# Kernel optimization log

Measured on AMD Instinct MI355X. Metric: run time of the kernel, lower is better.

Reference implementation:

```python
import jax, jax.numpy as jnp
import numpy as np

B, T, C, NH = 4, 2048, 1024, 16
HD = C // NH  # head dim = 64


def setup_inputs() -> dict:
    key = jax.random.key(0)
    k1, k2, k3 = jax.random.split(key, 3)
    x = jax.random.normal(k1, (B, T, C), dtype=jnp.float32)
    w_attn = jax.random.normal(k2, (C, 3 * C), dtype=jnp.float32) * (1.0 / np.sqrt(C))
    b_attn = jnp.zeros((3 * C,), dtype=jnp.float32)
    w_proj = jax.random.normal(k3, (C, C), dtype=jnp.float32) * (1.0 / np.sqrt(C))
    b_proj = jnp.zeros((C,), dtype=jnp.float32)
    return {"x": x, "w_attn": w_attn, "b_attn": b_attn, "w_proj": w_proj, "b_proj": b_proj}


def reference(x, w_attn, b_attn, w_proj, b_proj):
    Bx, Tx, Cx = x.shape
    # fused QKV projection
    qkv = x @ w_attn + b_attn              # [B, T, 3C]
    q, k, v = jnp.split(qkv, 3, axis=-1)   # each [B, T, C]
    # split heads: [B, NH, T, HD]
    q = q.reshape(Bx, Tx, NH, HD).transpose(0, 2, 1, 3)
    k = k.reshape(Bx, Tx, NH, HD).transpose(0, 2, 1, 3)
    v = v.reshape(Bx, Tx, NH, HD).transpose(0, 2, 1, 3)
    scale = 1.0 / np.sqrt(HD)
    att = jnp.einsum('bhqd,bhkd->bhqk', q, k) * scale  # [B, NH, T, T]
    causal = jnp.tril(jnp.ones((Tx, Tx), dtype=bool))
    att = jnp.where(causal[None, None], att, -jnp.inf)
    att = jax.nn.softmax(att, axis=-1)
    y = jnp.einsum('bhqk,bhkd->bhqd', att, v)           # [B, NH, T, HD]
    y = y.transpose(0, 2, 1, 3).reshape(Bx, Tx, Cx)
    return y @ w_proj + b_proj
```

## Files before the change

### kernel.cpp

```cpp
#include <hip/hip_runtime.h>
#include <hip/hip_bf16.h>

#define B_SZ 4
#define T_SZ 2048
#define C_SZ 1024
#define NH_SZ 16
#define HD_SZ 64
#define M_SZ (B_SZ * T_SZ)

typedef __bf16 bf16x8 __attribute__((ext_vector_type(8)));
typedef __bf16 bf16x4 __attribute__((ext_vector_type(4)));
typedef float f32x4 __attribute__((ext_vector_type(4)));

__device__ __forceinline__ void async_ld16(__hip_bfloat16* lds, const __hip_bfloat16* g) {
  __builtin_amdgcn_global_load_lds(
      (const __attribute__((address_space(1))) void*)g,
      (__attribute__((address_space(3))) void*)lds, 16, 0, 0);
}

__device__ __forceinline__ void bar() {
  asm volatile("" ::: "memory");
  __builtin_amdgcn_s_barrier();
  asm volatile("" ::: "memory");
}

__device__ __forceinline__ bf16x8 frag32(const __hip_bfloat16* base, int row, int q) {
  const int byte = (row << 6) + (((q ^ (row >> 1)) & 3) << 4);
  return *(const bf16x8*)((const char*)base + byte);
}

#define SWZ(row, cb) (((row) << 7) + ((cb) ^ (((row) & 7) << 4)))

__device__ __forceinline__ uint32_t pk2(float lo, float hi) {
  uint32_t r;
  asm("v_cvt_pk_bf16_f32 %0, %1, %2" : "=v"(r) : "v"(lo), "v"(hi));
  return r;
}

__global__ __launch_bounds__(256) void conv_bf16_kernel(
    const float* __restrict__ X, __hip_bfloat16* __restrict__ Y) {
  const int i = (blockIdx.x * 256 + threadIdx.x) * 4;
  float4 v = *(const float4*)&X[i];
  union { bf16x4 v; __hip_bfloat16 h[4]; } o;
  o.h[0] = __float2bfloat16(v.x); o.h[1] = __float2bfloat16(v.y);
  o.h[2] = __float2bfloat16(v.z); o.h[3] = __float2bfloat16(v.w);
  *(bf16x4*)&Y[i] = o.v;
}

template <int KD, int ND>
__global__ __launch_bounds__(256) void transpose_conv_kernel(
    const float* __restrict__ W, __hip_bfloat16* __restrict__ Wt) {
  __shared__ float sT[32][33];
  const int n0 = blockIdx.x * 32, k0 = blockIdx.y * 32;
  const int tid = threadIdx.x;
  {
    const int r = tid >> 3, c = (tid & 7) * 4;
    float4 v = *(const float4*)&W[(size_t)(k0 + r) * ND + n0 + c];
    sT[r][c] = v.x; sT[r][c + 1] = v.y; sT[r][c + 2] = v.z; sT[r][c + 3] = v.w;
  }
  __syncthreads();
  {
    const int n = tid >> 3, kq = (tid & 7) * 4;
    union { bf16x4 v; __hip_bfloat16 h[4]; } o;
#pragma unroll
    for (int j = 0; j < 4; ++j) o.h[j] = __float2bfloat16(sT[kq + j][n]);
    *(bf16x4*)&Wt[(size_t)(n0 + n) * KD + k0 + kq] = o.v;
  }
}


#define Q_PRESCALE 0.18033688011112042f

__global__ __launch_bounds__(512, 4) void gemm_qk_ring(
    const __hip_bfloat16* __restrict__ A, const __hip_bfloat16* __restrict__ Bt,
    const float* __restrict__ bias,
    __hip_bfloat16* __restrict__ qR, __hip_bfloat16* __restrict__ kR) {
  __shared__ __align__(16) __hip_bfloat16 sA[3][256 * 32];
  __shared__ __align__(16) __hip_bfloat16 sB[3][128 * 32];

  const int tid = threadIdx.x;
  const int wave = tid >> 6, lane = tid & 63;
  const int quad = lane >> 4, l16 = lane & 15;
  const int wm = wave >> 1, wn = wave & 1;

  const int xcd = (int)blockIdx.x & 7, lb = (int)blockIdx.x >> 3;
  const int bm = (xcd * 4 + (lb >> 4)) * 256;
  const int bn = (lb & 15) * 128;

  const int srow = tid >> 2;
  const int scol = 8 * ((tid & 3) ^ ((tid >> 3) & 3));
  const int sdst = tid * 8;
  const __hip_bfloat16* gA = A + (size_t)(bm + srow) * C_SZ + scol;
  const __hip_bfloat16* gB = Bt + (size_t)(bn + srow) * C_SZ + scol;

  f32x4 acc[4][4];
#pragma unroll
  for (int i = 0; i < 4; ++i)
#pragma unroll
    for (int j = 0; j < 4; ++j) acc[i][j] = (f32x4){0.f, 0.f, 0.f, 0.f};

#define STGQK(buf, kt)                                                         \
  do {                                                                         \
    async_ld16(&sA[buf][sdst], gA + (kt) * 32);                                \
    async_ld16(&sA[buf][4096 + sdst], gA + (size_t)128 * C_SZ + (kt) * 32);    \
    async_ld16(&sB[buf][sdst], gB + (kt) * 32);                                \
  } while (0)

  STGQK(0, 0);
  STGQK(1, 1);
  asm volatile("s_waitcnt vmcnt(3)" ::: "memory");
  bar();

  constexpr int NT = C_SZ / 32;
  int cur = 0;
  for (int kt = 0; kt < NT; ++kt) {
    const int stg = cur == 0 ? 2 : cur - 1;
    if (kt + 2 < NT) STGQK(stg, kt + 2);

    const __hip_bfloat16* ab = sA[cur];
    const __hip_bfloat16* bb = sB[cur];
    bf16x8 af[4], bfr[4];
#pragma unroll
    for (int mq = 0; mq < 4; ++mq) af[mq] = frag32(ab, wm * 64 + mq * 16 + l16, quad);
#pragma unroll
    for (int nq = 0; nq < 4; ++nq) bfr[nq] = frag32(bb, wn * 64 + nq * 16 + l16, quad);
#pragma unroll
    for (int mq = 0; mq < 4; ++mq)
#pragma unroll
      for (int nq = 0; nq < 4; ++nq)
        acc[mq][nq] = __builtin_amdgcn_mfma_f32_16x16x32_bf16(af[mq], bfr[nq], acc[mq][nq], 0, 0, 0);

    if (kt + 1 < NT) {
      if (kt + 2 < NT) asm volatile("s_waitcnt vmcnt(3)" ::: "memory");
      else             asm volatile("s_waitcnt vmcnt(0)" ::: "memory");
      bar();
    }
    cur = cur == 2 ? 0 : cur + 1;
  }
#undef STGQK

  float bv[4];
#pragma unroll
  for (int nq = 0; nq < 4; ++nq) bv[nq] = bias[bn + wn * 64 + nq * 16 + l16];
  const bool isQ = bn < C_SZ;
#pragma unroll
  for (int mq = 0; mq < 4; ++mq)
#pragma unroll
    for (int nq = 0; nq < 4; ++nq) {
      const int col = bn + wn * 64 + nq * 16 + l16;
      const int hh = (col >> 6) & 15, d = col & 63;
#pragma unroll
      for (int r = 0; r < 4; ++r) {
        const int row = bm + wm * 64 + mq * 16 + quad * 4 + r;
        const int bb_ = row >> 11, t = row & 2047;
        const size_t idx = ((size_t)(bb_ * 16 + hh) * T_SZ + t) * HD_SZ + d;
        const float val = acc[mq][nq][r] + bv[nq];
        if (isQ) qR[idx] = __float2bfloat16(val * Q_PRESCALE);
        else     kR[idx] = __float2bfloat16(val);
      }
    }
}

template <int MODE>
__global__ __launch_bounds__(256, 3) void gemm_tri128(
    const __hip_bfloat16* __restrict__ A, const __hip_bfloat16* __restrict__ Bt,
    const float* __restrict__ bias, float* __restrict__ Cf,
    __hip_bfloat16* __restrict__ vT) {
  __shared__ __align__(16) __hip_bfloat16 sA[3][128 * 32];
  __shared__ __align__(16) __hip_bfloat16 sB[3][128 * 32];

  const int tid = threadIdx.x;
  const int wave = tid >> 6, lane = tid & 63;
  const int quad = lane >> 4, l16 = lane & 15;
  const int rw = (wave & 1) * 64, cw = (wave >> 1) * 64;

  const int xcd = (int)blockIdx.x & 7, lb = (int)blockIdx.x >> 3;
  const int bm = (xcd * 8 + (lb >> 3)) * 128;
  const int bn = (lb & 7) * 128;

  const int srow = tid >> 2;
  const int scol = 8 * ((tid & 3) ^ ((tid >> 3) & 3));
  const int sdst = tid * 8;
  const __hip_bfloat16* gA = A + (size_t)(bm + srow) * C_SZ + scol;
  const __hip_bfloat16* gB = Bt + (size_t)(bn + srow) * C_SZ + scol;

  f32x4 acc[4][4];
#pragma unroll
  for (int i = 0; i < 4; ++i)
#pragma unroll
    for (int j = 0; j < 4; ++j) acc[i][j] = (f32x4){0.f, 0.f, 0.f, 0.f};

#define STG128(buf, kt)                                                        \
  do {                                                                         \
    async_ld16(&sA[buf][sdst], gA + (kt) * 32);                                \
    async_ld16(&sA[buf][2048 + sdst], gA + (size_t)64 * C_SZ + (kt) * 32);     \
    async_ld16(&sB[buf][sdst], gB + (kt) * 32);                                \
    async_ld16(&sB[buf][2048 + sdst], gB + (size_t)64 * C_SZ + (kt) * 32);     \
  } while (0)

  STG128(0, 0);
  STG128(1, 1);
  asm volatile("s_waitcnt vmcnt(4)" ::: "memory");
  bar();

  constexpr int NT = C_SZ / 32;
  int cur = 0;
  for (int kt = 0; kt < NT; ++kt) {
    const int stg = cur == 0 ? 2 : cur - 1;
    if (kt + 2 < NT) STG128(stg, kt + 2);

    const __hip_bfloat16* ab = sA[cur];
    const __hip_bfloat16* bb = sB[cur];
    bf16x8 af[4], bfr[4];
#pragma unroll
    for (int mq = 0; mq < 4; ++mq) af[mq] = frag32(ab, rw + mq * 16 + l16, quad);
#pragma unroll
    for (int nq = 0; nq < 4; ++nq) bfr[nq] = frag32(bb, cw + nq * 16 + l16, quad);
#pragma unroll
    for (int mq = 0; mq < 4; ++mq)
#pragma unroll
      for (int nq = 0; nq < 4; ++nq)
        acc[mq][nq] = __builtin_amdgcn_mfma_f32_16x16x32_bf16(af[mq], bfr[nq], acc[mq][nq], 0, 0, 0);

    if (kt + 1 < NT) {
      if (kt + 2 < NT) asm volatile("s_waitcnt vmcnt(4)" ::: "memory");
      else             asm volatile("s_waitcnt vmcnt(0)" ::: "memory");
      bar();
    }
    cur = cur == 2 ? 0 : cur + 1;
  }
#undef STG128

  float bv[4];
#pragma unroll
  for (int nq = 0; nq < 4; ++nq) bv[nq] = bias[bn + cw + nq * 16 + l16];
#pragma unroll
  for (int mq = 0; mq < 4; ++mq)
#pragma unroll
    for (int nq = 0; nq < 4; ++nq) {
      const int col = bn + cw + nq * 16 + l16;
#pragma unroll
      for (int r = 0; r < 4; ++r) {
        const int row = bm + rw + mq * 16 + quad * 4 + r;
        const float val = acc[mq][nq][r] + bv[nq];
        if (MODE == 0) {
          const int bb_ = row >> 11, t = row & 2047;
          const int hh = col >> 6, d = col & 63;
          vT[((size_t)(bb_ * 16 + hh) * HD_SZ + d) * T_SZ + t] = __float2bfloat16(val);
        } else {
          Cf[(size_t)row * C_SZ + col] = val;
        }
      }
    }
}


__device__ __forceinline__ void p_exchange(
    const f32x4& s0, const f32x4& s1, const f32x4& s2, const f32x4& s3,
    bool uSel, bool cSel, int srcE, int srcO, bf16x8& A0v, bf16x8& A1v) {
  uint32_t pk[4][2];
  pk[0][0] = pk2(s0[0], s0[1]); pk[0][1] = pk2(s0[2], s0[3]);
  pk[1][0] = pk2(s1[0], s1[1]); pk[1][1] = pk2(s1[2], s1[3]);
  pk[2][0] = pk2(s2[0], s2[1]); pk[2][1] = pk2(s2[2], s2[3]);
  pk[3][0] = pk2(s3[0], s3[1]); pk[3][1] = pk2(s3[2], s3[3]);

  uint32_t g0 = (uint32_t)__shfl((int)(uSel ? pk[1][0] : pk[0][0]), srcE, 64);
  uint32_t g1 = (uint32_t)__shfl((int)(uSel ? pk[0][0] : pk[1][0]), srcO, 64);
  uint32_t g2 = (uint32_t)__shfl((int)(uSel ? pk[3][0] : pk[2][0]), srcE, 64);
  uint32_t g3 = (uint32_t)__shfl((int)(uSel ? pk[2][0] : pk[3][0]), srcO, 64);
  uint32_t g4 = (uint32_t)__shfl((int)(uSel ? pk[1][1] : pk[0][1]), srcE, 64);
  uint32_t g5 = (uint32_t)__shfl((int)(uSel ? pk[0][1] : pk[1][1]), srcO, 64);
  uint32_t g6 = (uint32_t)__shfl((int)(uSel ? pk[3][1] : pk[2][1]), srcE, 64);
  uint32_t g7 = (uint32_t)__shfl((int)(uSel ? pk[2][1] : pk[3][1]), srcO, 64);

  union PU { uint32_t d[4]; bf16x8 v; } A0, A1;
  A0.d[0] = cSel ? g1 : g0;  A0.d[1] = cSel ? g5 : g4;
  A0.d[2] = cSel ? g0 : g1;  A0.d[3] = cSel ? g4 : g5;
  A1.d[0] = cSel ? g3 : g2;  A1.d[1] = cSel ? g7 : g6;
  A1.d[2] = cSel ? g2 : g3;  A1.d[3] = cSel ? g6 : g7;
  A0v = A0.v;
  A1v = A1.v;
}

__global__ __launch_bounds__(256, 3) void attn_mfma_kernel(
    const __hip_bfloat16* __restrict__ qR, const __hip_bfloat16* __restrict__ kR,
    const __hip_bfloat16* __restrict__ vT, __hip_bfloat16* __restrict__ y) {
  __shared__ __align__(16) __hip_bfloat16 sQ[128 * 64];
  __shared__ __align__(16) __hip_bfloat16 sK[64 * 64];
  __shared__ __align__(16) __hip_bfloat16 sVt[64 * 64];

  const int bh = blockIdx.x;
  const int tile = (int)gridDim.y - 1 - blockIdx.y;
  const int t0 = tile * 128;
  const int tid = threadIdx.x;
  const int wave = tid >> 6, lane = tid & 63;
  const int quad = lane >> 4, l16 = lane & 15;
  const int wrowQ = wave * 32;

  const __hip_bfloat16* qb = qR + (size_t)bh * T_SZ * HD_SZ;
  const __hip_bfloat16* kb = kR + (size_t)bh * T_SZ * HD_SZ;
  const __hip_bfloat16* vb = vT + (size_t)bh * HD_SZ * T_SZ;

  const int sr = tid >> 2;
  const int cb = 32 * (tid & 3);
  const int scE = (tid & 3) * 16;

  const bool uSel = (quad & 1) != 0;
  const bool cSel = (quad >> 1) != 0;
  const int srcE = l16 + 32 * (quad & 1) + 16 * (quad >> 1);
  const int srcO = srcE ^ 16;

  {
    const __hip_bfloat16* src = qb + (size_t)t0 * HD_SZ + tid * 16;
    *(float4*)((char*)sQ + SWZ(sr, cb)) = *(const float4*)src;
    *(float4*)((char*)sQ + SWZ(sr, cb + 16)) = *(const float4*)(src + 8);
    const __hip_bfloat16* src2 = src + 64 * HD_SZ;
    *(float4*)((char*)sQ + SWZ(64 + sr, cb)) = *(const float4*)src2;
    *(float4*)((char*)sQ + SWZ(64 + sr, cb + 16)) = *(const float4*)(src2 + 8);
  }

  float4 krg0, krg1, vrg0, vrg1;
  {
    const __hip_bfloat16* ks = kb + tid * 16;
    krg0 = *(const float4*)ks;
    krg1 = *(const float4*)(ks + 8);
    const __hip_bfloat16* vs = vb + (size_t)sr * T_SZ + scE;
    vrg0 = *(const float4*)vs;
    vrg1 = *(const float4*)(vs + 8);
  }

  __syncthreads();
  bf16x8 qa[2][2];
#pragma unroll
  for (int g = 0; g < 2; ++g) {
    const int qr = wrowQ + g * 16 + l16;
    qa[g][0] = *(const bf16x8*)((const char*)sQ + SWZ(qr, quad * 16));
    qa[g][1] = *(const bf16x8*)((const char*)sQ + SWZ(qr, 64 + quad * 16));
  }

  float lacc0 = 0.f, lacc1 = 0.f;
  f32x4 o[2][4];
#pragma unroll
  for (int g = 0; g < 2; ++g)
#pragma unroll
    for (int nn = 0; nn < 4; ++nn) o[g][nn] = (f32x4){0.f, 0.f, 0.f, 0.f};

  const int jmax = t0 + 64;
  for (int j0 = 0; j0 <= jmax; j0 += 64) {
    *(float4*)((char*)sK + SWZ(sr, cb)) = krg0;
    *(float4*)((char*)sK + SWZ(sr, cb + 16)) = krg1;
    *(float4*)((char*)sVt + SWZ(sr, cb)) = vrg0;
    *(float4*)((char*)sVt + SWZ(sr, cb + 16)) = vrg1;
    if (j0 + 64 <= jmax) {
      const __hip_bfloat16* ks = kb + (size_t)(j0 + 64) * HD_SZ + tid * 16;
      krg0 = *(const float4*)ks;
      krg1 = *(const float4*)(ks + 8);
      const __hip_bfloat16* vs = vb + (size_t)sr * T_SZ + j0 + 64 + scE;
      vrg0 = *(const float4*)vs;
      vrg1 = *(const float4*)(vs + 8);
    }
    __syncthreads();

    f32x4 s0[4], s1[4];
    __builtin_amdgcn_s_setprio(1);
#pragma unroll
    for (int sub = 0; sub < 4; ++sub) {
      const int kr = sub * 16 + l16;
      bf16x8 kf0 = *(const bf16x8*)((const char*)sK + SWZ(kr, quad * 16));
      bf16x8 kf1 = *(const bf16x8*)((const char*)sK + SWZ(kr, 64 + quad * 16));
      s0[sub] = (f32x4){0.f, 0.f, 0.f, 0.f};
      s0[sub] = __builtin_amdgcn_mfma_f32_16x16x32_bf16(kf0, qa[0][0], s0[sub], 0, 0, 0);
      s0[sub] = __builtin_amdgcn_mfma_f32_16x16x32_bf16(kf1, qa[0][1], s0[sub], 0, 0, 0);
      s1[sub] = (f32x4){0.f, 0.f, 0.f, 0.f};
      s1[sub] = __builtin_amdgcn_mfma_f32_16x16x32_bf16(kf0, qa[1][0], s1[sub], 0, 0, 0);
      s1[sub] = __builtin_amdgcn_mfma_f32_16x16x32_bf16(kf1, qa[1][1], s1[sub], 0, 0, 0);
    }
    __builtin_amdgcn_s_setprio(0);

    {
      const int qb0 = t0 + wrowQ;
      if (j0 + 63 > qb0) {
        const int qrow = qb0 + l16;
#pragma unroll
        for (int sub = 0; sub < 4; ++sub)
#pragma unroll
          for (int r = 0; r < 4; ++r)
            if (j0 + sub * 16 + quad * 4 + r > qrow) s0[sub][r] = -1e30f;
      }
      const int qb1 = qb0 + 16;
      if (j0 + 63 > qb1) {
        const int qrow = qb1 + l16;
#pragma unroll
        for (int sub = 0; sub < 4; ++sub)
#pragma unroll
          for (int r = 0; r < 4; ++r)
            if (j0 + sub * 16 + quad * 4 + r > qrow) s1[sub][r] = -1e30f;
      }
    }

#pragma unroll
    for (int sub = 0; sub < 4; ++sub)
#pragma unroll
      for (int r = 0; r < 4; ++r) {
        s0[sub][r] = __builtin_amdgcn_exp2f(s0[sub][r]);
        s1[sub][r] = __builtin_amdgcn_exp2f(s1[sub][r]);
      }
#pragma unroll
    for (int sub = 0; sub < 4; ++sub) {
      lacc0 += (s0[sub][0] + s0[sub][1]) + (s0[sub][2] + s0[sub][3]);
      lacc1 += (s1[sub][0] + s1[sub][1]) + (s1[sub][2] + s1[sub][3]);
    }

    bf16x8 A0g0, A1g0, A0g1, A1g1;
    p_exchange(s0[0], s0[1], s0[2], s0[3], uSel, cSel, srcE, srcO, A0g0, A1g0);
    p_exchange(s1[0], s1[1], s1[2], s1[3], uSel, cSel, srcE, srcO, A0g1, A1g1);

    __builtin_amdgcn_s_setprio(1);
#pragma unroll
    for (int nn = 0; nn < 4; ++nn) {
      const int vr = nn * 16 + l16;
      bf16x8 vf0 = *(const bf16x8*)((const char*)sVt + SWZ(vr, quad * 16));
      bf16x8 vf1 = *(const bf16x8*)((const char*)sVt + SWZ(vr, 64 + quad * 16));
      o[0][nn] = __builtin_amdgcn_mfma_f32_16x16x32_bf16(A0g0, vf0, o[0][nn], 0, 0, 0);
      o[0][nn] = __builtin_amdgcn_mfma_f32_16x16x32_bf16(A1g0, vf1, o[0][nn], 0, 0, 0);
      o[1][nn] = __builtin_amdgcn_mfma_f32_16x16x32_bf16(A0g1, vf0, o[1][nn], 0, 0, 0);
      o[1][nn] = __builtin_amdgcn_mfma_f32_16x16x32_bf16(A1g1, vf1, o[1][nn], 0, 0, 0);
    }
    __builtin_amdgcn_s_setprio(0);

    if (j0 < jmax) __syncthreads();
  }

  lacc0 += __shfl_xor(lacc0, 16);
  lacc0 += __shfl_xor(lacc0, 32);
  lacc1 += __shfl_xor(lacc1, 16);
  lacc1 += __shfl_xor(lacc1, 32);
  float inv[2][4];
#pragma unroll
  for (int r = 0; r < 4; ++r) {
    inv[0][r] = 1.0f / __shfl(lacc0, (lane & 48) + quad * 4 + r, 64);
    inv[1][r] = 1.0f / __shfl(lacc1, (lane & 48) + quad * 4 + r, 64);
  }

  const int b = bh >> 4, h = bh & 15;
#pragma unroll
  for (int g = 0; g < 2; ++g)
#pragma unroll
    for (int nn = 0; nn < 4; ++nn)
#pragma unroll
      for (int r = 0; r < 4; ++r) {
        const int t = t0 + wrowQ + g * 16 + quad * 4 + r;
        y[((size_t)b * T_SZ + t) * C_SZ + h * HD_SZ + nn * 16 + l16] =
            __float2bfloat16(o[g][nn][r] * inv[g][r]);
      }
}

extern "C" void kernel_launch(void* const* d_in, const int* in_sizes, int n_in,
                              void* d_out, int out_size, void* d_ws, size_t ws_size,
                              hipStream_t stream) {
  const float* x      = (const float*)d_in[0];
  const float* w_attn = (const float*)d_in[1];
  const float* b_attn = (const float*)d_in[2];
  const float* w_proj = (const float*)d_in[3];
  const float* b_proj = (const float*)d_in[4];
  float* out = (float*)d_out;

  __hip_bfloat16* xb  = (__hip_bfloat16*)d_ws;
  __hip_bfloat16* waT = xb + (size_t)M_SZ * C_SZ;
  __hip_bfloat16* wpT = waT + (size_t)3 * C_SZ * C_SZ;
  __hip_bfloat16* qR  = wpT + (size_t)C_SZ * C_SZ;
  __hip_bfloat16* kR  = qR + (size_t)M_SZ * C_SZ;
  __hip_bfloat16* vT  = kR + (size_t)M_SZ * C_SZ;
  __hip_bfloat16* yb  = xb;

  conv_bf16_kernel<<<(M_SZ * C_SZ) / (256 * 4), 256, 0, stream>>>(x, xb);
  transpose_conv_kernel<C_SZ, 3 * C_SZ><<<dim3(96, 32), 256, 0, stream>>>(w_attn, waT);
  transpose_conv_kernel<C_SZ, C_SZ><<<dim3(32, 32), 256, 0, stream>>>(w_proj, wpT);

  gemm_qk_ring<<<dim3(512), 512, 0, stream>>>(xb, waT, b_attn, qR, kR);

  gemm_tri128<0><<<dim3(512), 256, 0, stream>>>(
      xb, waT + (size_t)2 * C_SZ * C_SZ, b_attn + 2 * C_SZ, nullptr, vT);

  attn_mfma_kernel<<<dim3(B_SZ * NH_SZ, T_SZ / 128), 256, 0, stream>>>(qR, kR, vT, yb);

  gemm_tri128<1><<<dim3(512), 256, 0, stream>>>(
      (const __hip_bfloat16*)yb, wpT, b_proj, out, nullptr);
}
```

Before: 242.4 us.

## Enlarge attention query tile to 256 rows with per-wave causal skipping

The attention kernel now gives each block 256 query rows (64 per wave, four 16-row groups) in place of 128, so every K/V tile staged in LDS feeds twice as many MFMAs. Q fragments are loaded straight from global into registers, which removes the sQ LDS buffer and one barrier. Waves skip compute on key tiles that lie entirely above their causal diagonal. Tile order is remapped to interleave heavy and light tiles. In exchange, register pressure rises (occupancy hint drops from 3 to 2 blocks per CU), the grid halves, and waves within a block are imbalanced along the diagonal.

```diff
diff --git a/kernel.cpp b/kernel.cpp
--- a/kernel.cpp
+++ b/kernel.cpp
@@ -282,20 +282,20 @@
   A1v = A1.v;
 }
 
-__global__ __launch_bounds__(256, 3) void attn_mfma_kernel(
+__global__ __launch_bounds__(256, 2) void attn_mfma_kernel(
     const __hip_bfloat16* __restrict__ qR, const __hip_bfloat16* __restrict__ kR,
     const __hip_bfloat16* __restrict__ vT, __hip_bfloat16* __restrict__ y) {
-  __shared__ __align__(16) __hip_bfloat16 sQ[128 * 64];
   __shared__ __align__(16) __hip_bfloat16 sK[64 * 64];
   __shared__ __align__(16) __hip_bfloat16 sVt[64 * 64];
 
   const int bh = blockIdx.x;
-  const int tile = (int)gridDim.y - 1 - blockIdx.y;
-  const int t0 = tile * 128;
+  const int yy = (int)blockIdx.y;
+  const int tile = yy < 4 ? 7 - yy : yy - 4;
+  const int t0 = tile * 256;
   const int tid = threadIdx.x;
   const int wave = tid >> 6, lane = tid & 63;
   const int quad = lane >> 4, l16 = lane & 15;
-  const int wrowQ = wave * 32;
+  const int wrowQ = wave * 64;
 
   const __hip_bfloat16* qb = qR + (size_t)bh * T_SZ * HD_SZ;
   const __hip_bfloat16* kb = kR + (size_t)bh * T_SZ * HD_SZ;
@@ -310,13 +310,13 @@
   const int srcE = l16 + 32 * (quad & 1) + 16 * (quad >> 1);
   const int srcO = srcE ^ 16;
 
-  {
-    const __hip_bfloat16* src = qb + (size_t)t0 * HD_SZ + tid * 16;
-    *(float4*)((char*)sQ + SWZ(sr, cb)) = *(const float4*)src;
-    *(float4*)((char*)sQ + SWZ(sr, cb + 16)) = *(const float4*)(src + 8);
-    const __hip_bfloat16* src2 = src + 64 * HD_SZ;
-    *(float4*)((char*)sQ + SWZ(64 + sr, cb)) = *(const float4*)src2;
-    *(float4*)((char*)sQ + SWZ(64 + sr, cb + 16)) = *(const float4*)(src2 + 8);
+  bf16x8 qa[4][2];
+#pragma unroll
+  for (int g = 0; g < 4; ++g) {
+    const __hip_bfloat16* qrow =
+        qb + (size_t)(t0 + wrowQ + g * 16 + l16) * HD_SZ;
+    qa[g][0] = *(const bf16x8*)(qrow + quad * 8);
+    qa[g][1] = *(const bf16x8*)(qrow + 32 + quad * 8);
   }
 
   float4 krg0, krg1, vrg0, vrg1;
@@ -329,23 +329,17 @@
     vrg1 = *(const float4*)(vs + 8);
   }
 
-  __syncthreads();
-  bf16x8 qa[2][2];
-#pragma unroll
-  for (int g = 0; g < 2; ++g) {
-    const int qr = wrowQ + g * 16 + l16;
-    qa[g][0] = *(const bf16x8*)((const char*)sQ + SWZ(qr, quad * 16));
-    qa[g][1] = *(const bf16x8*)((const char*)sQ + SWZ(qr, 64 + quad * 16));
-  }
-
-  float lacc0 = 0.f, lacc1 = 0.f;
-  f32x4 o[2][4];
-#pragma unroll
-  for (int g = 0; g < 2; ++g)
+  float lacc[4];
+  f32x4 o[4][4];
+#pragma unroll
+  for (int g = 0; g < 4; ++g) {
+    lacc[g] = 0.f;
 #pragma unroll
     for (int nn = 0; nn < 4; ++nn) o[g][nn] = (f32x4){0.f, 0.f, 0.f, 0.f};
-
-  const int jmax = t0 + 64;
+  }
+
+  const int jmax = t0 + 192;
+  const int qmaxw = t0 + wrowQ + 63;
   for (int j0 = 0; j0 <= jmax; j0 += 64) {
     *(float4*)((char*)sK + SWZ(sr, cb)) = krg0;
     *(float4*)((char*)sK + SWZ(sr, cb + 16)) = krg1;
@@ -361,90 +355,87 @@
     }
     __syncthreads();
 
-    f32x4 s0[4], s1[4];
-    __builtin_amdgcn_s_setprio(1);
-#pragma unroll
-    for (int sub = 0; sub < 4; ++sub) {
-      const int kr = sub * 16 + l16;
-      bf16x8 kf0 = *(const bf16x8*)((const char*)sK + SWZ(kr, quad * 16));
-      bf16x8 kf1 = *(const bf16x8*)((const char*)sK + SWZ(kr, 64 + quad * 16));
-      s0[sub] = (f32x4){0.f, 0.f, 0.f, 0.f};
-      s0[sub] = __builtin_amdgcn_mfma_f32_16x16x32_bf16(kf0, qa[0][0], s0[sub], 0, 0, 0);
-      s0[sub] = __builtin_amdgcn_mfma_f32_16x16x32_bf16(kf1, qa[0][1], s0[sub], 0, 0, 0);
-      s1[sub] = (f32x4){0.f, 0.f, 0.f, 0.f};
-      s1[sub] = __builtin_amdgcn_mfma_f32_16x16x32_bf16(kf0, qa[1][0], s1[sub], 0, 0, 0);
-      s1[sub] = __builtin_amdgcn_mfma_f32_16x16x32_bf16(kf1, qa[1][1], s1[sub], 0, 0, 0);
-    }
-    __builtin_amdgcn_s_setprio(0);
-
-    {
-      const int qb0 = t0 + wrowQ;
-      if (j0 + 63 > qb0) {
-        const int qrow = qb0 + l16;
+    if (j0 <= qmaxw) {
+      f32x4 s[4][4];
+      __builtin_amdgcn_s_setprio(1);
+#pragma unroll
+      for (int sub = 0; sub < 4; ++sub) {
+        const int kr = sub * 16 + l16;
+        bf16x8 kf0 = *(const bf16x8*)((const char*)sK + SWZ(kr, quad * 16));
+        bf16x8 kf1 = *(const bf16x8*)((const char*)sK + SWZ(kr, 64 + quad * 16));
+#pragma unroll
+        for (int g = 0; g < 4; ++g) {
+          s[g][sub] = (f32x4){0.f, 0.f, 0.f, 0.f};
+          s[g][sub] = __builtin_amdgcn_mfma_f32_16x16x32_bf16(kf0, qa[g][0], s[g][sub], 0, 0, 0);
+          s[g][sub] = __builtin_amdgcn_mfma_f32_16x16x32_bf16(kf1, qa[g][1], s[g][sub], 0, 0, 0);
+        }
+      }
+      __builtin_amdgcn_s_setprio(0);
+
+#pragma unroll
+      for (int g = 0; g < 4; ++g) {
+        const int qbg = t0 + wrowQ + g * 16;
+        if (j0 + 63 > qbg) {
+          const int qrow = qbg + l16;
+#pragma unroll
+          for (int sub = 0; sub < 4; ++sub)
+#pragma unroll
+            for (int r = 0; r < 4; ++r)
+              if (j0 + sub * 16 + quad * 4 + r > qrow) s[g][sub][r] = -1e30f;
+        }
+      }
+
+#pragma unroll
+      for (int g = 0; g < 4; ++g) {
 #pragma unroll
         for (int sub = 0; sub < 4; ++sub)
 #pragma unroll
           for (int r = 0; r < 4; ++r)
-            if (j0 + sub * 16 + quad * 4 + r > qrow) s0[sub][r] = -1e30f;
-      }
-      const int qb1 = qb0 + 16;
-      if (j0 + 63 > qb1) {
-        const int qrow = qb1 + l16;
+            s[g][sub][r] = __builtin_amdgcn_exp2f(s[g][sub][r]);
 #pragma unroll
         for (int sub = 0; sub < 4; ++sub)
-#pragma unroll
-          for (int r = 0; r < 4; ++r)
-            if (j0 + sub * 16 + quad * 4 + r > qrow) s1[sub][r] = -1e30f;
-      }
-    }
-
-#pragma unroll
-    for (int sub = 0; sub < 4; ++sub)
-#pragma unroll
-      for (int r = 0; r < 4; ++r) {
-        s0[sub][r] = __builtin_amdgcn_exp2f(s0[sub][r]);
-        s1[sub][r] = __builtin_amdgcn_exp2f(s1[sub][r]);
-      }
-#pragma unroll
-    for (int sub = 0; sub < 4; ++sub) {
-      lacc0 += (s0[sub][0] + s0[sub][1]) + (s0[sub][2] + s0[sub][3]);
-      lacc1 += (s1[sub][0] + s1[sub][1]) + (s1[sub][2] + s1[sub][3]);
-    }
-
-    bf16x8 A0g0, A1g0, A0g1, A1g1;
-    p_exchange(s0[0], s0[1], s0[2], s0[3], uSel, cSel, srcE, srcO, A0g0, A1g0);
-    p_exchange(s1[0], s1[1], s1[2], s1[3], uSel, cSel, srcE, srcO, A0g1, A1g1);
-
-    __builtin_amdgcn_s_setprio(1);
-#pragma unroll
-    for (int nn = 0; nn < 4; ++nn) {
-      const int vr = nn * 16 + l16;
-      bf16x8 vf0 = *(const bf16x8*)((const char*)sVt + SWZ(vr, quad * 16));
-      bf16x8 vf1 = *(const bf16x8*)((const char*)sVt + SWZ(vr, 64 + quad * 16));
-      o[0][nn] = __builtin_amdgcn_mfma_f32_16x16x32_bf16(A0g0, vf0, o[0][nn], 0, 0, 0);
-      o[0][nn] = __builtin_amdgcn_mfma_f32_16x16x32_bf16(A1g0, vf1, o[0][nn], 0, 0, 0);
-      o[1][nn] = __builtin_amdgcn_mfma_f32_16x16x32_bf16(A0g1, vf0, o[1][nn], 0, 0, 0);
-      o[1][nn] = __builtin_amdgcn_mfma_f32_16x16x32_bf16(A1g1, vf1, o[1][nn], 0, 0, 0);
-    }
-    __builtin_amdgcn_s_setprio(0);
+          lacc[g] += (s[g][sub][0] + s[g][sub][1]) + (s[g][sub][2] + s[g][sub][3]);
+      }
+
+      bf16x8 A0[4], A1[4];
+#pragma unroll
+      for (int g = 0; g < 4; ++g)
+        p_exchange(s[g][0], s[g][1], s[g][2], s[g][3], uSel, cSel, srcE, srcO,
+                   A0[g], A1[g]);
+
+      __builtin_amdgcn_s_setprio(1);
+#pragma unroll
+      for (int nn = 0; nn < 4; ++nn) {
+        const int vr = nn * 16 + l16;
+        bf16x8 vf0 = *(const bf16x8*)((const char*)sVt + SWZ(vr, quad * 16));
+        bf16x8 vf1 = *(const bf16x8*)((const char*)sVt + SWZ(vr, 64 + quad * 16));
+#pragma unroll
+        for (int g = 0; g < 4; ++g) {
+          o[g][nn] = __builtin_amdgcn_mfma_f32_16x16x32_bf16(A0[g], vf0, o[g][nn], 0, 0, 0);
+          o[g][nn] = __builtin_amdgcn_mfma_f32_16x16x32_bf16(A1[g], vf1, o[g][nn], 0, 0, 0);
+        }
+      }
+      __builtin_amdgcn_s_setprio(0);
+    }
 
     if (j0 < jmax) __syncthreads();
   }
 
-  lacc0 += __shfl_xor(lacc0, 16);
-  lacc0 += __shfl_xor(lacc0, 32);
-  lacc1 += __shfl_xor(lacc1, 16);
-  lacc1 += __shfl_xor(lacc1, 32);
-  float inv[2][4];
-#pragma unroll
-  for (int r = 0; r < 4; ++r) {
-    inv[0][r] = 1.0f / __shfl(lacc0, (lane & 48) + quad * 4 + r, 64);
-    inv[1][r] = 1.0f / __shfl(lacc1, (lane & 48) + quad * 4 + r, 64);
-  }
+#pragma unroll
+  for (int g = 0; g < 4; ++g) {
+    lacc[g] += __shfl_xor(lacc[g], 16);
+    lacc[g] += __shfl_xor(lacc[g], 32);
+  }
+  float inv[4][4];
+#pragma unroll
+  for (int g = 0; g < 4; ++g)
+#pragma unroll
+    for (int r = 0; r < 4; ++r)
+      inv[g][r] = 1.0f / __shfl(lacc[g], (lane & 48) + quad * 4 + r, 64);
 
   const int b = bh >> 4, h = bh & 15;
 #pragma unroll
-  for (int g = 0; g < 2; ++g)
+  for (int g = 0; g < 4; ++g)
 #pragma unroll
     for (int nn = 0; nn < 4; ++nn)
 #pragma unroll
@@ -482,7 +473,7 @@
   gemm_tri128<0><<<dim3(512), 256, 0, stream>>>(
       xb, waT + (size_t)2 * C_SZ * C_SZ, b_attn + 2 * C_SZ, nullptr, vT);
 
-  attn_mfma_kernel<<<dim3(B_SZ * NH_SZ, T_SZ / 128), 256, 0, stream>>>(qR, kR, vT, yb);
+  attn_mfma_kernel<<<dim3(B_SZ * NH_SZ, T_SZ / 256), 256, 0, stream>>>(qR, kR, vT, yb);
 
   gemm_tri128<1><<<dim3(512), 256, 0, stream>>>(
       (const __hip_bfloat16*)yb, wpT, b_proj, out, nullptr);
```

Result: slower. 252.2 us (+4.0%).

## Merge prep kernels and fuse Q/K/V projections into one 128x128 GEMM launch

Applied to the files above, without the earlier changes.

Folds the x conversion and the two weight transpose-convert kernels into a single prep_kernel that dispatches on block index. It also replaces the separate 256x128 QK GEMM and the 128x128 V GEMM with one 128x128 tiled QKV GEMM of 1536 blocks, which routes its epilogue to the Q, K or transposed V layout. The aim is fewer launches and less tail inefficiency between the stages. In exchange, QK tiles drop from 256 to 128 rows, which lowers operand reuse per block.

```diff
diff --git a/kernel.cpp b/kernel.cpp
--- a/kernel.cpp
+++ b/kernel.cpp
@@ -37,22 +37,38 @@
   return r;
 }
 
-__global__ __launch_bounds__(256) void conv_bf16_kernel(
-    const float* __restrict__ X, __hip_bfloat16* __restrict__ Y) {
-  const int i = (blockIdx.x * 256 + threadIdx.x) * 4;
-  float4 v = *(const float4*)&X[i];
-  union { bf16x4 v; __hip_bfloat16 h[4]; } o;
-  o.h[0] = __float2bfloat16(v.x); o.h[1] = __float2bfloat16(v.y);
-  o.h[2] = __float2bfloat16(v.z); o.h[3] = __float2bfloat16(v.w);
-  *(bf16x4*)&Y[i] = o.v;
-}
-
-template <int KD, int ND>
-__global__ __launch_bounds__(256) void transpose_conv_kernel(
-    const float* __restrict__ W, __hip_bfloat16* __restrict__ Wt) {
+#define Q_PRESCALE 0.18033688011112042f
+
+__global__ __launch_bounds__(256) void prep_kernel(
+    const float* __restrict__ x, const float* __restrict__ w_attn,
+    const float* __restrict__ w_proj, __hip_bfloat16* __restrict__ xb,
+    __hip_bfloat16* __restrict__ waT, __hip_bfloat16* __restrict__ wpT) {
   __shared__ float sT[32][33];
-  const int n0 = blockIdx.x * 32, k0 = blockIdx.y * 32;
+  const int bid = blockIdx.x;
   const int tid = threadIdx.x;
+
+  if (bid < 8192) {
+    const int i = (bid * 256 + tid) * 4;
+    float4 v = *(const float4*)&x[i];
+    union { bf16x4 v; __hip_bfloat16 h[4]; } o;
+    o.h[0] = __float2bfloat16(v.x); o.h[1] = __float2bfloat16(v.y);
+    o.h[2] = __float2bfloat16(v.z); o.h[3] = __float2bfloat16(v.w);
+    *(bf16x4*)&xb[i] = o.v;
+    return;
+  }
+
+  const float* W;
+  __hip_bfloat16* Wt;
+  int ND, n0, k0;
+  if (bid < 8192 + 3072) {
+    const int id = bid - 8192;
+    W = w_attn; Wt = waT; ND = 3 * C_SZ;
+    n0 = (id % 96) * 32; k0 = (id / 96) * 32;
+  } else {
+    const int id = bid - 11264;
+    W = w_proj; Wt = wpT; ND = C_SZ;
+    n0 = (id % 32) * 32; k0 = (id / 32) * 32;
+  }
   {
     const int r = tid >> 3, c = (tid & 7) * 4;
     float4 v = *(const float4*)&W[(size_t)(k0 + r) * ND + n0 + c];
@@ -64,28 +80,27 @@
     union { bf16x4 v; __hip_bfloat16 h[4]; } o;
 #pragma unroll
     for (int j = 0; j < 4; ++j) o.h[j] = __float2bfloat16(sT[kq + j][n]);
-    *(bf16x4*)&Wt[(size_t)(n0 + n) * KD + k0 + kq] = o.v;
-  }
-}
-
-
-#define Q_PRESCALE 0.18033688011112042f
-
-__global__ __launch_bounds__(512, 4) void gemm_qk_ring(
+    *(bf16x4*)&Wt[(size_t)(n0 + n) * C_SZ + k0 + kq] = o.v;
+  }
+}
+
+__global__ __launch_bounds__(256, 3) void gemm_qkv128(
     const __hip_bfloat16* __restrict__ A, const __hip_bfloat16* __restrict__ Bt,
     const float* __restrict__ bias,
-    __hip_bfloat16* __restrict__ qR, __hip_bfloat16* __restrict__ kR) {
-  __shared__ __align__(16) __hip_bfloat16 sA[3][256 * 32];
+    __hip_bfloat16* __restrict__ qR, __hip_bfloat16* __restrict__ kR,
+    __hip_bfloat16* __restrict__ vT) {
+  __shared__ __align__(16) __hip_bfloat16 sA[3][128 * 32];
   __shared__ __align__(16) __hip_bfloat16 sB[3][128 * 32];
 
   const int tid = threadIdx.x;
   const int wave = tid >> 6, lane = tid & 63;
   const int quad = lane >> 4, l16 = lane & 15;
-  const int wm = wave >> 1, wn = wave & 1;
+  const int rw = (wave & 1) * 64, cw = (wave >> 1) * 64;
 
   const int xcd = (int)blockIdx.x & 7, lb = (int)blockIdx.x >> 3;
-  const int bm = (xcd * 4 + (lb >> 4)) * 256;
-  const int bn = (lb & 15) * 128;
+  const int region = lb / 64, rr = lb % 64;
+  const int bm = (xcd * 8 + (rr >> 3)) * 128;
+  const int bn = (region * 8 + (rr & 7)) * 128;
 
   const int srow = tid >> 2;
   const int scol = 8 * ((tid & 3) ^ ((tid >> 3) & 3));
@@ -99,98 +114,7 @@
 #pragma unroll
     for (int j = 0; j < 4; ++j) acc[i][j] = (f32x4){0.f, 0.f, 0.f, 0.f};
 
-#define STGQK(buf, kt)                                                         \
-  do {                                                                         \
-    async_ld16(&sA[buf][sdst], gA + (kt) * 32);                                \
-    async_ld16(&sA[buf][4096 + sdst], gA + (size_t)128 * C_SZ + (kt) * 32);    \
-    async_ld16(&sB[buf][sdst], gB + (kt) * 32);                                \
-  } while (0)
-
-  STGQK(0, 0);
-  STGQK(1, 1);
-  asm volatile("s_waitcnt vmcnt(3)" ::: "memory");
-  bar();
-
-  constexpr int NT = C_SZ / 32;
-  int cur = 0;
-  for (int kt = 0; kt < NT; ++kt) {
-    const int stg = cur == 0 ? 2 : cur - 1;
-    if (kt + 2 < NT) STGQK(stg, kt + 2);
-
-    const __hip_bfloat16* ab = sA[cur];
-    const __hip_bfloat16* bb = sB[cur];
-    bf16x8 af[4], bfr[4];
-#pragma unroll
-    for (int mq = 0; mq < 4; ++mq) af[mq] = frag32(ab, wm * 64 + mq * 16 + l16, quad);
-#pragma unroll
-    for (int nq = 0; nq < 4; ++nq) bfr[nq] = frag32(bb, wn * 64 + nq * 16 + l16, quad);
-#pragma unroll
-    for (int mq = 0; mq < 4; ++mq)
-#pragma unroll
-      for (int nq = 0; nq < 4; ++nq)
-        acc[mq][nq] = __builtin_amdgcn_mfma_f32_16x16x32_bf16(af[mq], bfr[nq], acc[mq][nq], 0, 0, 0);
-
-    if (kt + 1 < NT) {
-      if (kt + 2 < NT) asm volatile("s_waitcnt vmcnt(3)" ::: "memory");
-      else             asm volatile("s_waitcnt vmcnt(0)" ::: "memory");
-      bar();
-    }
-    cur = cur == 2 ? 0 : cur + 1;
-  }
-#undef STGQK
-
-  float bv[4];
-#pragma unroll
-  for (int nq = 0; nq < 4; ++nq) bv[nq] = bias[bn + wn * 64 + nq * 16 + l16];
-  const bool isQ = bn < C_SZ;
-#pragma unroll
-  for (int mq = 0; mq < 4; ++mq)
-#pragma unroll
-    for (int nq = 0; nq < 4; ++nq) {
-      const int col = bn + wn * 64 + nq * 16 + l16;
-      const int hh = (col >> 6) & 15, d = col & 63;
-#pragma unroll
-      for (int r = 0; r < 4; ++r) {
-        const int row = bm + wm * 64 + mq * 16 + quad * 4 + r;
-        const int bb_ = row >> 11, t = row & 2047;
-        const size_t idx = ((size_t)(bb_ * 16 + hh) * T_SZ + t) * HD_SZ + d;
-        const float val = acc[mq][nq][r] + bv[nq];
-        if (isQ) qR[idx] = __float2bfloat16(val * Q_PRESCALE);
-        else     kR[idx] = __float2bfloat16(val);
-      }
-    }
-}
-
-template <int MODE>
-__global__ __launch_bounds__(256, 3) void gemm_tri128(
-    const __hip_bfloat16* __restrict__ A, const __hip_bfloat16* __restrict__ Bt,
-    const float* __restrict__ bias, float* __restrict__ Cf,
-    __hip_bfloat16* __restrict__ vT) {
-  __shared__ __align__(16) __hip_bfloat16 sA[3][128 * 32];
-  __shared__ __align__(16) __hip_bfloat16 sB[3][128 * 32];
-
-  const int tid = threadIdx.x;
-  const int wave = tid >> 6, lane = tid & 63;
-  const int quad = lane >> 4, l16 = lane & 15;
-  const int rw = (wave & 1) * 64, cw = (wave >> 1) * 64;
-
-  const int xcd = (int)blockIdx.x & 7, lb = (int)blockIdx.x >> 3;
-  const int bm = (xcd * 8 + (lb >> 3)) * 128;
-  const int bn = (lb & 7) * 128;
-
-  const int srow = tid >> 2;
-  const int scol = 8 * ((tid & 3) ^ ((tid >> 3) & 3));
-  const int sdst = tid * 8;
-  const __hip_bfloat16* gA = A + (size_t)(bm + srow) * C_SZ + scol;
-  const __hip_bfloat16* gB = Bt + (size_t)(bn + srow) * C_SZ + scol;
-
-  f32x4 acc[4][4];
-#pragma unroll
-  for (int i = 0; i < 4; ++i)
-#pragma unroll
-    for (int j = 0; j < 4; ++j) acc[i][j] = (f32x4){0.f, 0.f, 0.f, 0.f};
-
-#define STG128(buf, kt)                                                        \
+#define STG(buf, kt)                                                           \
   do {                                                                         \
     async_ld16(&sA[buf][sdst], gA + (kt) * 32);                                \
     async_ld16(&sA[buf][2048 + sdst], gA + (size_t)64 * C_SZ + (kt) * 32);     \
@@ -198,8 +122,8 @@
     async_ld16(&sB[buf][2048 + sdst], gB + (size_t)64 * C_SZ + (kt) * 32);     \
   } while (0)
 
-  STG128(0, 0);
-  STG128(1, 1);
+  STG(0, 0);
+  STG(1, 1);
   asm volatile("s_waitcnt vmcnt(4)" ::: "memory");
   bar();
 
@@ -207,7 +131,7 @@
   int cur = 0;
   for (int kt = 0; kt < NT; ++kt) {
     const int stg = cur == 0 ? 2 : cur - 1;
-    if (kt + 2 < NT) STG128(stg, kt + 2);
+    if (kt + 2 < NT) STG(stg, kt + 2);
 
     const __hip_bfloat16* ab = sA[cur];
     const __hip_bfloat16* bb = sB[cur];
@@ -229,27 +153,116 @@
     }
     cur = cur == 2 ? 0 : cur + 1;
   }
-#undef STG128
+#undef STG
 
   float bv[4];
 #pragma unroll
   for (int nq = 0; nq < 4; ++nq) bv[nq] = bias[bn + cw + nq * 16 + l16];
+  const bool isQ = bn < C_SZ;
+  const bool isK = !isQ && bn < 2 * C_SZ;
 #pragma unroll
   for (int mq = 0; mq < 4; ++mq)
 #pragma unroll
     for (int nq = 0; nq < 4; ++nq) {
       const int col = bn + cw + nq * 16 + l16;
+      const int hh = (col >> 6) & 15, d = col & 63;
 #pragma unroll
       for (int r = 0; r < 4; ++r) {
         const int row = bm + rw + mq * 16 + quad * 4 + r;
+        const int bb_ = row >> 11, t = row & 2047;
+        const int bh64 = bb_ * 16 + hh;
         const float val = acc[mq][nq][r] + bv[nq];
-        if (MODE == 0) {
-          const int bb_ = row >> 11, t = row & 2047;
-          const int hh = col >> 6, d = col & 63;
-          vT[((size_t)(bb_ * 16 + hh) * HD_SZ + d) * T_SZ + t] = __float2bfloat16(val);
+        if (isQ) {
+          qR[((size_t)bh64 * T_SZ + t) * HD_SZ + d] = __float2bfloat16(val * Q_PRESCALE);
+        } else if (isK) {
+          kR[((size_t)bh64 * T_SZ + t) * HD_SZ + d] = __float2bfloat16(val);
         } else {
-          Cf[(size_t)row * C_SZ + col] = val;
+          vT[((size_t)bh64 * HD_SZ + d) * T_SZ + t] = __float2bfloat16(val);
         }
+      }
+    }
+}
+
+__global__ __launch_bounds__(256, 3) void gemm_proj128(
+    const __hip_bfloat16* __restrict__ A, const __hip_bfloat16* __restrict__ Bt,
+    const float* __restrict__ bias, float* __restrict__ Cf) {
+  __shared__ __align__(16) __hip_bfloat16 sA[3][128 * 32];
+  __shared__ __align__(16) __hip_bfloat16 sB[3][128 * 32];
+
+  const int tid = threadIdx.x;
+  const int wave = tid >> 6, lane = tid & 63;
+  const int quad = lane >> 4, l16 = lane & 15;
+  const int rw = (wave & 1) * 64, cw = (wave >> 1) * 64;
+
+  const int xcd = (int)blockIdx.x & 7, lb = (int)blockIdx.x >> 3;
+  const int bm = (xcd * 8 + (lb >> 3)) * 128;
+  const int bn = (lb & 7) * 128;
+
+  const int srow = tid >> 2;
+  const int scol = 8 * ((tid & 3) ^ ((tid >> 3) & 3));
+  const int sdst = tid * 8;
+  const __hip_bfloat16* gA = A + (size_t)(bm + srow) * C_SZ + scol;
+  const __hip_bfloat16* gB = Bt + (size_t)(bn + srow) * C_SZ + scol;
+
+  f32x4 acc[4][4];
+#pragma unroll
+  for (int i = 0; i < 4; ++i)
+#pragma unroll
+    for (int j = 0; j < 4; ++j) acc[i][j] = (f32x4){0.f, 0.f, 0.f, 0.f};
+
+#define STG(buf, kt)                                                           \
+  do {                                                                         \
+    async_ld16(&sA[buf][sdst], gA + (kt) * 32);                                \
+    async_ld16(&sA[buf][2048 + sdst], gA + (size_t)64 * C_SZ + (kt) * 32);     \
+    async_ld16(&sB[buf][sdst], gB + (kt) * 32);                                \
+    async_ld16(&sB[buf][2048 + sdst], gB + (size_t)64 * C_SZ + (kt) * 32);     \
+  } while (0)
+
+  STG(0, 0);
+  STG(1, 1);
+  asm volatile("s_waitcnt vmcnt(4)" ::: "memory");
+  bar();
+
+  constexpr int NT = C_SZ / 32;
+  int cur = 0;
+  for (int kt = 0; kt < NT; ++kt) {
+    const int stg = cur == 0 ? 2 : cur - 1;
+    if (kt + 2 < NT) STG(stg, kt + 2);
+
+    const __hip_bfloat16* ab = sA[cur];
+    const __hip_bfloat16* bb = sB[cur];
+    bf16x8 af[4], bfr[4];
+#pragma unroll
+    for (int mq = 0; mq < 4; ++mq) af[mq] = frag32(ab, rw + mq * 16 + l16, quad);
+#pragma unroll
+    for (int nq = 0; nq < 4; ++nq) bfr[nq] = frag32(bb, cw + nq * 16 + l16, quad);
+#pragma unroll
+    for (int mq = 0; mq < 4; ++mq)
+#pragma unroll
+      for (int nq = 0; nq < 4; ++nq)
+        acc[mq][nq] = __builtin_amdgcn_mfma_f32_16x16x32_bf16(af[mq], bfr[nq], acc[mq][nq], 0, 0, 0);
+
+    if (kt + 1 < NT) {
+      if (kt + 2 < NT) asm volatile("s_waitcnt vmcnt(4)" ::: "memory");
+      else             asm volatile("s_waitcnt vmcnt(0)" ::: "memory");
+      bar();
+    }
+    cur = cur == 2 ? 0 : cur + 1;
+  }
+#undef STG
+
+  float bv[4];
+#pragma unroll
+  for (int nq = 0; nq < 4; ++nq) bv[nq] = bias[bn + cw + nq * 16 + l16];
+#pragma unroll
+  for (int mq = 0; mq < 4; ++mq)
+#pragma unroll
+    for (int nq = 0; nq < 4; ++nq) {
+      const int col = bn + cw + nq * 16 + l16;
+#pragma unroll
+      for (int r = 0; r < 4; ++r) {
+        const int row = bm + rw + mq * 16 + quad * 4 + r;
+        Cf[(size_t)row * C_SZ + col] = acc[mq][nq][r] + bv[nq];
       }
     }
 }
@@ -473,17 +486,11 @@
   __hip_bfloat16* vT  = kR + (size_t)M_SZ * C_SZ;
   __hip_bfloat16* yb  = xb;
 
-  conv_bf16_kernel<<<(M_SZ * C_SZ) / (256 * 4), 256, 0, stream>>>(x, xb);
-  transpose_conv_kernel<C_SZ, 3 * C_SZ><<<dim3(96, 32), 256, 0, stream>>>(w_attn, waT);
-  transpose_conv_kernel<C_SZ, C_SZ><<<dim3(32, 32), 256, 0, stream>>>(w_proj, wpT);
-
-  gemm_qk_ring<<<dim3(512), 512, 0, stream>>>(xb, waT, b_attn, qR, kR);
-
-  gemm_tri128<0><<<dim3(512), 256, 0, stream>>>(
-      xb, waT + (size_t)2 * C_SZ * C_SZ, b_attn + 2 * C_SZ, nullptr, vT);
+  prep_kernel<<<dim3(12288), 256, 0, stream>>>(x, w_attn, w_proj, xb, waT, wpT);
+
+  gemm_qkv128<<<dim3(1536), 256, 0, stream>>>(xb, waT, b_attn, qR, kR, vT);
 
   attn_mfma_kernel<<<dim3(B_SZ * NH_SZ, T_SZ / 128), 256, 0, stream>>>(qR, kR, vT, yb);
 
-  gemm_tri128<1><<<dim3(512), 256, 0, stream>>>(
-      (const __hip_bfloat16*)yb, wpT, b_proj, out, nullptr);
-}
+  gemm_proj128<<<dim3(512), 256, 0, stream>>>(yb, wpT, b_proj, out);
+}
```

Result: slower. 251.2 us (+3.6%).
